# Performance work log

Measured on AMD Instinct MI355X. Metric: run time of the kernel, lower is better.

Reference implementation:

```python
import jax, jax.numpy as jnp
import numpy as np

LOG_2PI = float(np.log(2.0 * np.pi))


def kde_self_log_prob(X, sigma):
    """log prob of each row of X under a KDE whose components are all rows of X.

    Matches tfd.MixtureSameFamily(Categorical(uniform), MVNDiag(loc=X, scale=sigma)):
      log p(q) = logsumexp_i [ -0.5*||q - X_i||^2/sigma^2 - d*log(sigma) - d/2*log(2pi) ] - log(N)
    """
    n, d = X.shape
    sq = jnp.sum(X * X, axis=1)  # [N]
    # pairwise squared distances [N, N]; clamp tiny negatives from cancellation
    d2 = jnp.maximum(sq[:, None] + sq[None, :] - 2.0 * (X @ X.T), 0.0)
    log_comp = -0.5 * d2 / (sigma * sigma) - d * jnp.log(sigma) - 0.5 * d * LOG_2PI
    return jax.nn.logsumexp(log_comp, axis=1) - jnp.log(jnp.asarray(n, X.dtype))


def setup_inputs() -> dict:
    key = jax.random.key(0)
    kx, ky = jax.random.split(key)
    N, D = 8192, 128
    latent_x = jax.random.normal(kx, (N, D), dtype=jnp.float32)
    latent_y = jax.random.normal(ky, (N, D), dtype=jnp.float32)
    # learned bandwidth parameters (tf.Variable scalars, init 1.0)
    sigma_joint = jnp.float32(1.0)
    sigma_x = jnp.float32(1.0)
    sigma_y = jnp.float32(1.0)
    return {"latent_x": latent_x, "latent_y": latent_y,
            "sigma_joint": sigma_joint, "sigma_x": sigma_x, "sigma_y": sigma_y}


def reference(latent_x, latent_y, sigma_joint, sigma_x, sigma_y):
    latent_joint = jnp.concatenate([latent_x, latent_y], axis=1)  # [N, 2d]
    lp_joint = kde_self_log_prob(latent_joint, sigma_joint)  # [N]
    lp_x = kde_self_log_prob(latent_x, sigma_x)              # [N]
    lp_y = kde_self_log_prob(latent_y, sigma_y)              # [N]
    I_xy = jnp.exp(lp_joint) * (lp_joint - (lp_x + lp_y))
    return -jnp.sum(I_xy)
```

## Files before the change

kernel.cpp:

```cpp
#include <hip/hip_runtime.h>
#include <hip/hip_bf16.h>
#include <math.h>

#define NROW 8192
#define DD   128

#define V12BLK  512
#define V12NBLK 512
#define NRANKV8 8128

#define NT   64
#define TS   128
#define NPAIR 2080
#define FBLOCK 512

#define LOG_2PI 1.8378770664093453f
#define L2E     1.4426950408889634f
#define FP_SCALE 1099511627776.0

typedef __attribute__((ext_vector_type(8))) short bf16x8;
typedef __attribute__((ext_vector_type(4))) float f32x4;

#define SQX_B 0
#define SQY_B 32768
#define BSUM_B 65536
#define XB_B  65792
#define YB_B  (XB_B + NROW*DD*2)
#define TS_B  (YB_B + NROW*DD*2)
#define COLV8_B  TS_B
#define ROWSV8_B (COLV8_B + NRANKV8*192*4)
#define PS_B     (ROWSV8_B + 2048*192*4)
#define V8_NEED  (PS_B + 128*8*192*4)
#define ACC_B TS_B

__device__ __forceinline__ unsigned short f2bf(float f) {
    unsigned int x = __float_as_uint(f);
    unsigned int r = (x + 0x7fffu + ((x >> 16) & 1u)) >> 16;
    return (unsigned short)r;
}
__device__ __forceinline__ float fexp2(float x) { return __builtin_amdgcn_exp2f(x); }
__device__ __forceinline__ int rank_v8(int I, int J) {
    return I * 127 - (I * (I - 1)) / 2 + (J - I - 1);
}

template <bool PRE>
__global__ void sq_kernel(const float* __restrict__ X, const float* __restrict__ Y,
                          float* __restrict__ sqx, float* __restrict__ sqy,
                          unsigned short* __restrict__ XB, unsigned short* __restrict__ YB) {
    int tid  = threadIdx.x;
    int rowg = blockIdx.x * 8 + (tid >> 5);
    int lane = tid & 31;
    bool isX = rowg < NROW;
    const float* src = isX ? (X + (size_t)rowg * DD) : (Y + (size_t)(rowg - NROW) * DD);
    float4 v = reinterpret_cast<const float4*>(src)[lane];
    if (PRE) {
        unsigned int w0 = (unsigned int)f2bf(v.x) | ((unsigned int)f2bf(v.y) << 16);
        unsigned int w1 = (unsigned int)f2bf(v.z) | ((unsigned int)f2bf(v.w) << 16);
        unsigned short* dst = (isX ? XB + (size_t)rowg * DD
                                   : YB + (size_t)(rowg - NROW) * DD) + lane * 4;
        uint2 pk; pk.x = w0; pk.y = w1;
        *reinterpret_cast<uint2*>(dst) = pk;
    }
    float s = v.x * v.x + v.y * v.y + v.z * v.z + v.w * v.w;
#pragma unroll
    for (int m = 16; m; m >>= 1) s += __shfl_xor(s, m, 64);
    if (lane == 0) { if (isX) sqx[rowg] = s; else sqy[rowg - NROW] = s; }
}

template <bool SAME, bool DIAG>
__device__ __forceinline__ void combine_v8(const f32x4 (&ax)[4], const f32x4 (&ay)[4],
                                           const float* __restrict__ sqi0,
                                           const float* __restrict__ sqi1,
                                           float bxp, float byp,
                                           float cx2, float cy2, float m2cx, float m2cy,
                                           float rx, float ry,
                                           float (&prow)[4][4][3], float (&pcol)[3],
                                           int lane, int wql) {
    const int coll = wql * 16 + (lane & 15);
#pragma unroll
    for (int rf = 0; rf < 4; ++rf) {
        const int rb = rf * 16 + ((lane >> 4) << 2);
        f32x4 sixv = *reinterpret_cast<const f32x4*>(&sqi0[rb]);
        f32x4 siyv = *reinterpret_cast<const f32x4*>(&sqi1[rb]);
#pragma unroll
        for (int reg = 0; reg < 4; ++reg) {
            float tx = fmaf(ax[rf][reg], m2cx, fmaf(cx2, sixv[reg], bxp));
            float ty = fmaf(ay[rf][reg], m2cy, fmaf(cy2, siyv[reg], byp));
            float ex = fexp2(tx);
            float ey = fexp2(ty);
            float ej = SAME ? (ex * ey) : fexp2(fmaf(tx, rx, ty * ry));
            if (DIAG) {
                bool dg = (rb + reg) == coll;
                ex = dg ? 1.f : ex;  ey = dg ? 1.f : ey;  ej = dg ? 1.f : ej;
            }
            prow[rf][reg][0] += ex; prow[rf][reg][1] += ey; prow[rf][reg][2] += ej;
            pcol[0] += ex;          pcol[1] += ey;          pcol[2] += ej;
        }
    }
}

__launch_bounds__(V12BLK, 1)
__global__ void kde_v12(const unsigned short* __restrict__ XB,
                        const unsigned short* __restrict__ YB,
                        const float* __restrict__ sjp, const float* __restrict__ sxp,
                        const float* __restrict__ syp,
                        const float* __restrict__ sqx, const float* __restrict__ sqy,
                        float* __restrict__ COL, float* __restrict__ ROWS) {
    __shared__ unsigned short A[2][64][DD];
    __shared__ float sqi[2][64];
    __shared__ float rowred[8][64][3];

    const int tid  = threadIdx.x;
    const int lane = tid & 63;
    const int wq   = tid >> 6;
    const int wg   = wq >> 2;
    const int wql  = wq & 3;

    const int bid = blockIdx.x;
    const int cch = bid & 7;
    const int p   = bid >> 3;
    const int t0  = (129 * cch) >> 3;
    const int t1  = (129 * (cch + 1)) >> 3;
    const int nJA = 128 - p;

    const float sxv = *sxp, syv = *syp, sjv = *sjp;
    const float cx2 = -0.5f * L2E / (sxv * sxv);
    const float cy2 = -0.5f * L2E / (syv * syv);
    const float cj2 = -0.5f * L2E / (sjv * sjv);
    const bool  same = (cx2 == cy2) && (cy2 == cj2);
    const float m2cx = -2.f * cx2, m2cy = -2.f * cy2;
    const float rx = cj2 / cx2, ry = cj2 / cy2;

    float prow[4][4][3];
#pragma unroll
    for (int a = 0; a < 4; ++a)
#pragma unroll
        for (int b = 0; b < 4; ++b)
#pragma unroll
            for (int c = 0; c < 3; ++c) prow[a][b][c] = 0.f;

    int  prevWhich = -1;
    bool wrote0 = false, wrote1 = false;

    const int e1 = (t1 < nJA) ? t1 : nJA;
    const int s0 = (t0 > nJA) ? t0 : nJA;

    for (int band = 0; band < 2; ++band) {
        int I, Jf, cnt;
        if (band == 0) { I = p;       Jf = p + t0;  cnt = e1 - t0; }
        else           { I = 127 - p; Jf = s0 - 1;  cnt = t1 - s0; }
        if (cnt <= 0) continue;

        __syncthreads();
        if (prevWhich >= 0) {
#pragma unroll
            for (int rf = 0; rf < 4; ++rf)
#pragma unroll
                for (int reg = 0; reg < 4; ++reg)
#pragma unroll
                    for (int ch = 0; ch < 3; ++ch) {
                        float v = prow[rf][reg][ch];
                        v += __shfl_xor(v, 1, 64);
                        v += __shfl_xor(v, 2, 64);
                        v += __shfl_xor(v, 4, 64);
                        v += __shfl_xor(v, 8, 64);
                        if ((lane & 15) == 0)
                            rowred[wq][rf * 16 + ((lane >> 4) << 2) + reg][ch] = v;
                        prow[rf][reg][ch] = 0.f;
                    }
        }
        {
            int mat = wq >> 2;
            int g   = tid & 255;
            const unsigned short* gb = (mat ? YB : XB) + (size_t)(I * 64) * DD;
#pragma unroll
            for (int i = 0; i < 4; ++i) {
                int e    = g + i * 256;
                int row  = e >> 4;
                int col8 = e & 15;
                uint4 v = *reinterpret_cast<const uint4*>(gb + (size_t)row * DD + col8 * 8);
                int sl = col8 ^ (row & 7);
                *reinterpret_cast<uint4*>(&A[mat][row][sl * 8]) = v;
            }
        }
        if (tid < 128) sqi[tid >> 6][tid & 63] = ((tid < 64) ? sqx : sqy)[I * 64 + (tid & 63)];
        __syncthreads();
        if (prevWhich >= 0 && tid < 192) {
            int ch = tid >> 6, row = tid & 63;
            size_t slot = ((size_t)(p * 8 + cch) * 2 + prevWhich);
            float v = 0.f;
#pragma unroll
            for (int w = 0; w < 8; ++w) v += rowred[w][row][ch];
            ROWS[(slot * 3 + ch) * 64 + row] = v;
        }
        if (prevWhich == 0) wrote0 = true; else if (prevWhich == 1) wrote1 = true;
        prevWhich = (I == p) ? 0 : 1;

        for (int s = 0; s < cnt; s += 2) {
            const int  so    = s + wg;
            const bool valid = so < cnt;
            if (!valid) continue;
            const int J    = Jf + so;
            const bool diag = (I == J);
            const int colg = J * 64 + wql * 16 + (lane & 15);
            const float bxp = cx2 * sqx[colg];
            const float byp = cy2 * sqy[colg];

            f32x4 ax[4], ay[4];
#pragma unroll
            for (int rf = 0; rf < 4; ++rf) {
                ax[rf] = (f32x4){0.f, 0.f, 0.f, 0.f};
                ay[rf] = (f32x4){0.f, 0.f, 0.f, 0.f};
            }
#pragma unroll 2
            for (int kk = 0; kk < 4; ++kk) {
                bf16x8 bfx, bfy, afx[4], afy[4];
                {
                    size_t off = (size_t)colg * DD + kk * 32 + (lane >> 4) * 8;
                    bfx = *reinterpret_cast<const bf16x8*>(XB + off);
                    bfy = *reinterpret_cast<const bf16x8*>(YB + off);
                }
#pragma unroll
                for (int rf = 0; rf < 4; ++rf) {
                    int r  = rf * 16 + (lane & 15);
                    int sl = (kk * 4 + (lane >> 4)) ^ (r & 7);
                    afx[rf] = *reinterpret_cast<const bf16x8*>(&A[0][r][sl * 8]);
                    afy[rf] = *reinterpret_cast<const bf16x8*>(&A[1][r][sl * 8]);
                }
#pragma unroll
                for (int rf = 0; rf < 4; ++rf) {
                    ax[rf] = __builtin_amdgcn_mfma_f32_16x16x32_bf16(afx[rf], bfx, ax[rf], 0, 0, 0);
                    ay[rf] = __builtin_amdgcn_mfma_f32_16x16x32_bf16(afy[rf], bfy, ay[rf], 0, 0, 0);
                }
            }

            float pcol[3] = {0.f, 0.f, 0.f};
            if (same) { if (diag) combine_v8<true , true >(ax, ay, &sqi[0][0], &sqi[1][0], bxp, byp, cx2, cy2, m2cx, m2cy, rx, ry, prow, pcol, lane, wql);
                        else      combine_v8<true , false>(ax, ay, &sqi[0][0], &sqi[1][0], bxp, byp, cx2, cy2, m2cx, m2cy, rx, ry, prow, pcol, lane, wql); }
            else      { if (diag) combine_v8<false, true >(ax, ay, &sqi[0][0], &sqi[1][0], bxp, byp, cx2, cy2, m2cx, m2cy, rx, ry, prow, pcol, lane, wql);
                        else      combine_v8<false, false>(ax, ay, &sqi[0][0], &sqi[1][0], bxp, byp, cx2, cy2, m2cx, m2cy, rx, ry, prow, pcol, lane, wql); }

            if (!diag) {
                int rank = rank_v8(I, J);
#pragma unroll
                for (int ch = 0; ch < 3; ++ch) {
                    float v = pcol[ch];
                    v += __shfl_xor(v, 16, 64);
                    v += __shfl_xor(v, 32, 64);
                    if (lane < 16)
                        COL[((size_t)rank * 3 + ch) * 64 + wql * 16 + lane] = v;
                }
            }
        }
    }

    __syncthreads();
#pragma unroll
    for (int rf = 0; rf < 4; ++rf)
#pragma unroll
        for (int reg = 0; reg < 4; ++reg)
#pragma unroll
            for (int ch = 0; ch < 3; ++ch) {
                float v = prow[rf][reg][ch];
                v += __shfl_xor(v, 1, 64);
                v += __shfl_xor(v, 2, 64);
                v += __shfl_xor(v, 4, 64);
                v += __shfl_xor(v, 8, 64);
                if ((lane & 15) == 0)
                    rowred[wq][rf * 16 + ((lane >> 4) << 2) + reg][ch] = v;
            }
    __syncthreads();
    if (tid < 192) {
        int ch = tid >> 6, row = tid & 63;
        size_t slot = ((size_t)(p * 8 + cch) * 2 + prevWhich);
        float v = 0.f;
#pragma unroll
        for (int w = 0; w < 8; ++w) v += rowred[w][row][ch];
        ROWS[(slot * 3 + ch) * 64 + row] = v;
    }
    if (prevWhich == 0) wrote0 = true; else wrote1 = true;
    if (!wrote0 && tid < 192) {
        int ch = tid >> 6, row = tid & 63;
        ROWS[(((size_t)(p * 8 + cch) * 2 + 0) * 3 + ch) * 64 + row] = 0.f;
    }
    if (!wrote1 && tid < 192) {
        int ch = tid >> 6, row = tid & 63;
        ROWS[(((size_t)(p * 8 + cch) * 2 + 1) * 3 + ch) * 64 + row] = 0.f;
    }
}

__global__ void colsum_v8(const float* __restrict__ COL, float* __restrict__ PS) {
    const int J = blockIdx.x;
    const int s = blockIdx.y;
    const int t = threadIdx.x;
    const int i0 = (J * s) >> 3;
    const int i1 = (J * (s + 1)) >> 3;
    float v = 0.f;
    for (int I = i0; I < i1; ++I)
        v += COL[(size_t)rank_v8(I, J) * 192 + t];
    PS[((size_t)J * 8 + s) * 192 + t] = v;
}

__global__ void lp_v12(const float* __restrict__ sjp, const float* __restrict__ sxp,
                       const float* __restrict__ syp,
                       const float* __restrict__ PS, const float* __restrict__ ROWS,
                       float* __restrict__ bsum) {
    int b = blockIdx.x;
    int t = threadIdx.x;
    int r = b * 128 + t;
    int Ib = r >> 6;
    int c  = r & 63;
    float S0 = 0.f, S1 = 0.f, S2 = 0.f;
    {
        int p = (Ib < 64) ? Ib : 127 - Ib;
        int which = (Ib < 64) ? 0 : 1;
        for (int ch8 = 0; ch8 < 8; ++ch8) {
            size_t slot = ((size_t)(p * 8 + ch8) * 2 + which) * 3;
            S0 += ROWS[(slot + 0) * 64 + c];
            S1 += ROWS[(slot + 1) * 64 + c];
            S2 += ROWS[(slot + 2) * 64 + c];
        }
    }
    for (int s = 0; s < 8; ++s) {
        size_t base = ((size_t)Ib * 8 + s) * 192 + c;
        S0 += PS[base];
        S1 += PS[base + 64];
        S2 += PS[base + 128];
    }
    float sx = *sxp, sy = *syp, sj = *sjp;
    float logN = logf((float)NROW);
    float lpx = logf(S0) - (float)DD * logf(sx) - 0.5f * (float)DD * LOG_2PI - logN;
    float lpy = logf(S1) - (float)DD * logf(sy) - 0.5f * (float)DD * LOG_2PI - logN;
    float lpj = logf(S2) - 2.0f * (float)DD * logf(sj) - (float)DD * LOG_2PI - logN;
    float I_ = expf(lpj) * (lpj - lpx - lpy);
#pragma unroll
    for (int m = 1; m < 64; m <<= 1) I_ += __shfl_xor(I_, m, 64);
    __shared__ float w0s[2];
    if ((t & 63) == 0) w0s[t >> 6] = I_;
    __syncthreads();
    if (t == 0) bsum[b] = w0s[0] + w0s[1];
}

__global__ void final_reduce(const float* __restrict__ bsum, float* __restrict__ out) {
    int t = threadIdx.x;
    float v = bsum[t];
#pragma unroll
    for (int m = 1; m < 64; m <<= 1) v += __shfl_xor(v, m, 64);
    if (t == 0) out[0] = -v;
}

template <bool SAME>
__device__ __forceinline__ void fb_combine(const f32x4 (&ax)[4][2], const f32x4 (&ay)[4][2],
                                           const float (&sq)[4][TS],
                                           float (&rowred)[4][TS][3], float (&colred)[2][TS][3],
                                           int wr, int wc, int lane,
                                           float cx2, float cy2, float cj2) {
    float pcol[2][3] = {{0.f,0.f,0.f},{0.f,0.f,0.f}};
#pragma unroll
    for (int rf = 0; rf < 4; ++rf) {
        float prow[4][3] = {{0.f,0.f,0.f},{0.f,0.f,0.f},{0.f,0.f,0.f},{0.f,0.f,0.f}};
        float sxi[4], syi[4];
#pragma unroll
        for (int reg = 0; reg < 4; ++reg) {
            int row = wr*64 + rf*16 + ((lane>>4)<<2) + reg;
            sxi[reg] = sq[0][row]; syi[reg] = sq[1][row];
        }
#pragma unroll
        for (int cf = 0; cf < 2; ++cf) {
            int col = wc*32 + cf*16 + (lane & 15);
            float qx = sq[2][col], qy = sq[3][col];
#pragma unroll
            for (int reg = 0; reg < 4; ++reg) {
                float gx = ax[rf][cf][reg], gy = ay[rf][cf][reg];
                float d2x = fmaxf(fmaf(-2.f, gx, sxi[reg] + qx), 0.f);
                float d2y = fmaxf(fmaf(-2.f, gy, syi[reg] + qy), 0.f);
                float ex = fexp2(d2x * cx2);
                float ey = fexp2(d2y * cy2);
                float ej = SAME ? (ex * ey) : fexp2(fmaf(d2y, cj2, d2x * cj2));
                prow[reg][0] += ex; prow[reg][1] += ey; prow[reg][2] += ej;
                pcol[cf][0]  += ex; pcol[cf][1]  += ey; pcol[cf][2]  += ej;
            }
        }
#pragma unroll
        for (int reg = 0; reg < 4; ++reg)
#pragma unroll
            for (int ch = 0; ch < 3; ++ch) {
                float v = prow[reg][ch];
                v += __shfl_xor(v, 1, 64); v += __shfl_xor(v, 2, 64);
                v += __shfl_xor(v, 4, 64); v += __shfl_xor(v, 8, 64);
                if ((lane & 15) == 0)
                    rowred[wc][wr*64 + rf*16 + ((lane>>4)<<2) + reg][ch] = v;
            }
    }
#pragma unroll
    for (int cf = 0; cf < 2; ++cf)
#pragma unroll
        for (int ch = 0; ch < 3; ++ch) {
            float v = pcol[cf][ch];
            v += __shfl_xor(v, 16, 64); v += __shfl_xor(v, 32, 64);
            if (lane < 16) colred[wr][wc*32 + cf*16 + lane][ch] = v;
        }
}

__launch_bounds__(FBLOCK)
__global__ void kde_fb(const float* __restrict__ X, const float* __restrict__ Y,
                       const float* __restrict__ sjp, const float* __restrict__ sxp,
                       const float* __restrict__ syp,
                       unsigned long long* __restrict__ acc,
                       const float* __restrict__ sqx, const float* __restrict__ sqy) {
    __shared__ unsigned short T[4][TS][DD];
    __shared__ float sq[4][TS];
    __shared__ float rowred[4][TS][3];
    __shared__ float colred[2][TS][3];

    const int tid  = threadIdx.x;
    const int lane = tid & 63;
    const int wid  = tid >> 6;
    const int wr   = wid >> 2;
    const int wc   = wid & 3;

    int b = (blockIdx.x & 7) * (NPAIR / 8) + (blockIdx.x >> 3);
    int ti = 0, rem = b;
    while (rem >= NT - ti) { rem -= NT - ti; ++ti; }
    int tj = ti + rem;
    const int i0 = ti * TS, j0 = tj * TS;

    const float sxv = *sxp, syv = *syp, sjv = *sjp;
    const float cx2 = -0.5f * L2E / (sxv * sxv);
    const float cy2 = -0.5f * L2E / (syv * syv);
    const float cj2 = -0.5f * L2E / (sjv * sjv);
    const bool samesig = (cx2 == cy2) && (cy2 == cj2);

    for (int c = tid; c < 8192; c += FBLOCK) {
        int t = c >> 11, row = (c >> 4) & 127, col8 = c & 15;
        const float* base =
            (t == 0) ? X + (size_t)i0 * DD : (t == 1) ? Y + (size_t)i0 * DD :
            (t == 2) ? X + (size_t)j0 * DD : Y + (size_t)j0 * DD;
        const float4* s4 = reinterpret_cast<const float4*>(base + row * DD + col8 * 8);
        float4 a = s4[0], bb = s4[1];
        unsigned int w0 = (unsigned int)f2bf(a.x)  | ((unsigned int)f2bf(a.y)  << 16);
        unsigned int w1 = (unsigned int)f2bf(a.z)  | ((unsigned int)f2bf(a.w)  << 16);
        unsigned int w2 = (unsigned int)f2bf(bb.x) | ((unsigned int)f2bf(bb.y) << 16);
        unsigned int w3 = (unsigned int)f2bf(bb.z) | ((unsigned int)f2bf(bb.w) << 16);
        uint4 pk = make_uint4(w0, w1, w2, w3);
        int sl = (col8 ^ (row & 7)) << 3;
        *reinterpret_cast<uint4*>(&T[t][row][sl]) = pk;
    }
    {
        int t = tid >> 7, r = tid & 127;
        const float* s = (t == 0) ? sqx + i0 : (t == 1) ? sqy + i0
                       : (t == 2) ? sqx + j0 : sqy + j0;
        sq[t][r] = s[r];
    }
    __syncthreads();

    f32x4 ax[4][2], ay[4][2];
#pragma unroll
    for (int rf = 0; rf < 4; ++rf)
#pragma unroll
        for (int cf = 0; cf < 2; ++cf) {
            ax[rf][cf] = (f32x4){0.f,0.f,0.f,0.f};
            ay[rf][cf] = (f32x4){0.f,0.f,0.f,0.f};
        }
#pragma unroll
    for (int kk = 0; kk < 4; ++kk) {
        const int k0 = kk * 4 + (lane >> 4);
        bf16x8 afx[4], afy[4], bfx[2], bfy[2];
#pragma unroll
        for (int rf = 0; rf < 4; ++rf) {
            int r  = wr * 64 + rf * 16 + (lane & 15);
            int sl = (k0 ^ (r & 7)) << 3;
            afx[rf] = *reinterpret_cast<const bf16x8*>(&T[0][r][sl]);
            afy[rf] = *reinterpret_cast<const bf16x8*>(&T[1][r][sl]);
        }
#pragma unroll
        for (int cf = 0; cf < 2; ++cf) {
            int r  = wc * 32 + cf * 16 + (lane & 15);
            int sl = (k0 ^ (r & 7)) << 3;
            bfx[cf] = *reinterpret_cast<const bf16x8*>(&T[2][r][sl]);
            bfy[cf] = *reinterpret_cast<const bf16x8*>(&T[3][r][sl]);
        }
#pragma unroll
        for (int rf = 0; rf < 4; ++rf)
#pragma unroll
            for (int cf = 0; cf < 2; ++cf) {
                ax[rf][cf] = __builtin_amdgcn_mfma_f32_16x16x32_bf16(afx[rf], bfx[cf], ax[rf][cf], 0, 0, 0);
                ay[rf][cf] = __builtin_amdgcn_mfma_f32_16x16x32_bf16(afy[rf], bfy[cf], ay[rf][cf], 0, 0, 0);
            }
    }

    if (samesig) fb_combine<true >(ax, ay, sq, rowred, colred, wr, wc, lane, cx2, cy2, cj2);
    else         fb_combine<false>(ax, ay, sq, rowred, colred, wr, wc, lane, cx2, cy2, cj2);
    __syncthreads();

    if (tid < TS) {
        int r = tid;
#pragma unroll
        for (int ch = 0; ch < 3; ++ch) {
            float v = rowred[0][r][ch] + rowred[1][r][ch] + rowred[2][r][ch] + rowred[3][r][ch];
            atomicAdd(&acc[(size_t)(i0 + r) * 3 + ch],
                      (unsigned long long)(long long)((double)v * FP_SCALE));
        }
    } else if (tid < 2 * TS && ti != tj) {
        int r = tid - TS;
#pragma unroll
        for (int ch = 0; ch < 3; ++ch) {
            float v = colred[0][r][ch] + colred[1][r][ch];
            atomicAdd(&acc[(size_t)(j0 + r) * 3 + ch],
                      (unsigned long long)(long long)((double)v * FP_SCALE));
        }
    }
}

__global__ void lp_fb(const float* __restrict__ sjp, const float* __restrict__ sxp,
                      const float* __restrict__ syp,
                      const unsigned long long* __restrict__ acc,
                      float* __restrict__ bsum) {
    int b = blockIdx.x, t = threadIdx.x;
    size_t row = (size_t)b * 128 + t;
    const double INV = 1.0 / FP_SCALE;
    float S0 = (float)((double)acc[row * 3 + 0] * INV);
    float S1 = (float)((double)acc[row * 3 + 1] * INV);
    float S2 = (float)((double)acc[row * 3 + 2] * INV);
    float sx = *sxp, sy = *syp, sj = *sjp;
    float logN = logf((float)NROW);
    float lpx = logf(S0) - (float)DD * logf(sx) - 0.5f * (float)DD * LOG_2PI - logN;
    float lpy = logf(S1) - (float)DD * logf(sy) - 0.5f * (float)DD * LOG_2PI - logN;
    float lpj = logf(S2) - 2.0f * (float)DD * logf(sj) - (float)DD * LOG_2PI - logN;
    float I = expf(lpj) * (lpj - lpx - lpy);
#pragma unroll
    for (int m = 1; m < 64; m <<= 1) I += __shfl_xor(I, m, 64);
    __shared__ float w0[2];
    if ((t & 63) == 0) w0[t >> 6] = I;
    __syncthreads();
    if (t == 0) bsum[b] = w0[0] + w0[1];
}

extern "C" void kernel_launch(void* const* d_in, const int* in_sizes, int n_in,
                              void* d_out, int out_size, void* d_ws, size_t ws_size,
                              hipStream_t stream) {
    (void)in_sizes; (void)n_in; (void)out_size;
    const float* X  = (const float*)d_in[0];
    const float* Y  = (const float*)d_in[1];
    const float* sj = (const float*)d_in[2];
    const float* sx = (const float*)d_in[3];
    const float* sy = (const float*)d_in[4];
    float* out = (float*)d_out;
    char*  w   = (char*)d_ws;

    float* SQX  = (float*)(w + SQX_B);
    float* SQY  = (float*)(w + SQY_B);
    float* BSUM = (float*)(w + BSUM_B);
    unsigned short* XB = (unsigned short*)(w + XB_B);
    unsigned short* YB = (unsigned short*)(w + YB_B);

    if (ws_size >= (size_t)V8_NEED) {
        float* COLS = (float*)(w + COLV8_B);
        float* ROWS = (float*)(w + ROWSV8_B);
        float* PS   = (float*)(w + PS_B);
        sq_kernel<true ><<<dim3(2048), dim3(256), 0, stream>>>(X, Y, SQX, SQY, XB, YB);
        kde_v12<<<dim3(V12NBLK), dim3(V12BLK), 0, stream>>>(XB, YB, sj, sx, sy, SQX, SQY, COLS, ROWS);
        colsum_v8<<<dim3(128, 8), dim3(192), 0, stream>>>(COLS, PS);
        lp_v12<<<dim3(64), dim3(128), 0, stream>>>(sj, sx, sy, PS, ROWS, BSUM);
    } else {
        unsigned long long* ACC = (unsigned long long*)(w + ACC_B);
        hipMemsetAsync(w + ACC_B, 0, NROW * 3 * sizeof(unsigned long long), stream);
        sq_kernel<false><<<dim3(2048), dim3(256), 0, stream>>>(X, Y, SQX, SQY, XB, YB);
        kde_fb<<<dim3(NPAIR), dim3(FBLOCK), 0, stream>>>(X, Y, sj, sx, sy, ACC, SQX, SQY);
        lp_fb<<<dim3(64), dim3(128), 0, stream>>>(sj, sx, sy, ACC, BSUM);
    }
    final_reduce<<<dim3(1), dim3(64), 0, stream>>>(BSUM, out);
}
```

Baseline: 89.38 us.

## Switch pairwise KDE tiles to 32x32x16 bf16 MFMA with atomic column sums

The main pairwise kernel now computes each 64x64 tile as four 32x32 quadrants using 32x32x16 bf16 MFMA instructions instead of sixteen 16x16x32 MFMAs per wave. This cuts B-fragment and LDS loads per accumulated element and changes the row and column partial-sum layout. Two waves now cover each column block, so column partials go to COL through atomicAdd, which requires a new memset of the COL buffer before launch. The exchange is extra atomics and a memset, plus a different register footprint.

```diff
diff --git a/kernel.cpp b/kernel.cpp
--- a/kernel.cpp
+++ b/kernel.cpp
@@ -5,8 +5,8 @@
 #define NROW 8192
 #define DD   128
 
-#define V12BLK  512
-#define V12NBLK 512
+#define V13BLK  512
+#define V13NBLK 512
 #define NRANKV8 8128
 
 #define NT   64
@@ -18,8 +18,9 @@
 #define L2E     1.4426950408889634f
 #define FP_SCALE 1099511627776.0
 
-typedef __attribute__((ext_vector_type(8))) short bf16x8;
-typedef __attribute__((ext_vector_type(4))) float f32x4;
+typedef __attribute__((ext_vector_type(8)))  short bf16x8;
+typedef __attribute__((ext_vector_type(4)))  float f32x4;
+typedef __attribute__((ext_vector_type(16))) float f32x16;
 
 #define SQX_B 0
 #define SQY_B 32768
@@ -67,40 +68,41 @@
     if (lane == 0) { if (isX) sqx[rowg] = s; else sqy[rowg - NROW] = s; }
 }
 
+
 template <bool SAME, bool DIAG>
-__device__ __forceinline__ void combine_v8(const f32x4 (&ax)[4], const f32x4 (&ay)[4],
-                                           const float* __restrict__ sqi0,
-                                           const float* __restrict__ sqi1,
-                                           float bxp, float byp,
-                                           float cx2, float cy2, float m2cx, float m2cy,
-                                           float rx, float ry,
-                                           float (&prow)[4][4][3], float (&pcol)[3],
-                                           int lane, int wql) {
-    const int coll = wql * 16 + (lane & 15);
-#pragma unroll
-    for (int rf = 0; rf < 4; ++rf) {
-        const int rb = rf * 16 + ((lane >> 4) << 2);
-        f32x4 sixv = *reinterpret_cast<const f32x4*>(&sqi0[rb]);
-        f32x4 siyv = *reinterpret_cast<const f32x4*>(&sqi1[rb]);
-#pragma unroll
-        for (int reg = 0; reg < 4; ++reg) {
-            float tx = fmaf(ax[rf][reg], m2cx, fmaf(cx2, sixv[reg], bxp));
-            float ty = fmaf(ay[rf][reg], m2cy, fmaf(cy2, siyv[reg], byp));
+__device__ __forceinline__ void combine_v13(const f32x16& axv, const f32x16& ayv,
+                                            const float* __restrict__ sq0,
+                                            const float* __restrict__ sq1,
+                                            float bxp, float byp,
+                                            float cx2, float cy2, float m2cx, float m2cy,
+                                            float rx, float ry,
+                                            int qr, int qc, int hi, int c32,
+                                            float (&prow)[16][3], float (&pcol)[3]) {
+#pragma unroll
+    for (int q = 0; q < 4; ++q) {
+        const int rb = qr * 32 + q * 8 + hi * 4;
+        f32x4 sixv = *reinterpret_cast<const f32x4*>(&sq0[rb]);
+        f32x4 siyv = *reinterpret_cast<const f32x4*>(&sq1[rb]);
+#pragma unroll
+        for (int m = 0; m < 4; ++m) {
+            const int reg = q * 4 + m;
+            float tx = fmaf(axv[reg], m2cx, fmaf(cx2, sixv[m], bxp));
+            float ty = fmaf(ayv[reg], m2cy, fmaf(cy2, siyv[m], byp));
             float ex = fexp2(tx);
             float ey = fexp2(ty);
             float ej = SAME ? (ex * ey) : fexp2(fmaf(tx, rx, ty * ry));
             if (DIAG) {
-                bool dg = (rb + reg) == coll;
+                bool dg = (qr == qc) && ((q * 8 + hi * 4 + m) == c32);
                 ex = dg ? 1.f : ex;  ey = dg ? 1.f : ey;  ej = dg ? 1.f : ej;
             }
-            prow[rf][reg][0] += ex; prow[rf][reg][1] += ey; prow[rf][reg][2] += ej;
-            pcol[0] += ex;          pcol[1] += ey;          pcol[2] += ej;
-        }
-    }
-}
-
-__launch_bounds__(V12BLK, 1)
-__global__ void kde_v12(const unsigned short* __restrict__ XB,
+            prow[reg][0] += ex; prow[reg][1] += ey; prow[reg][2] += ej;
+            pcol[0] += ex;      pcol[1] += ey;      pcol[2] += ej;
+        }
+    }
+}
+
+__launch_bounds__(V13BLK, 1)
+__global__ void kde_v13(const unsigned short* __restrict__ XB,
                         const unsigned short* __restrict__ YB,
                         const float* __restrict__ sjp, const float* __restrict__ sxp,
                         const float* __restrict__ syp,
@@ -108,13 +110,17 @@
                         float* __restrict__ COL, float* __restrict__ ROWS) {
     __shared__ unsigned short A[2][64][DD];
     __shared__ float sqi[2][64];
-    __shared__ float rowred[8][64][3];
+    __shared__ float rowred[8][32][3];
 
     const int tid  = threadIdx.x;
     const int lane = tid & 63;
     const int wq   = tid >> 6;
     const int wg   = wq >> 2;
     const int wql  = wq & 3;
+    const int qr   = wql >> 1;
+    const int qc   = wql & 1;
+    const int hi   = lane >> 5;
+    const int c32  = lane & 31;
 
     const int bid = blockIdx.x;
     const int cch = bid & 7;
@@ -131,13 +137,11 @@
     const float m2cx = -2.f * cx2, m2cy = -2.f * cy2;
     const float rx = cj2 / cx2, ry = cj2 / cy2;
 
-    float prow[4][4][3];
-#pragma unroll
-    for (int a = 0; a < 4; ++a)
-#pragma unroll
-        for (int b = 0; b < 4; ++b)
-#pragma unroll
-            for (int c = 0; c < 3; ++c) prow[a][b][c] = 0.f;
+    float prow[16][3];
+#pragma unroll
+    for (int a = 0; a < 16; ++a)
+#pragma unroll
+        for (int c = 0; c < 3; ++c) prow[a][c] = 0.f;
 
     int  prevWhich = -1;
     bool wrote0 = false, wrote1 = false;
@@ -154,19 +158,20 @@
         __syncthreads();
         if (prevWhich >= 0) {
 #pragma unroll
-            for (int rf = 0; rf < 4; ++rf)
-#pragma unroll
-                for (int reg = 0; reg < 4; ++reg)
+            for (int q = 0; q < 4; ++q)
+#pragma unroll
+                for (int m = 0; m < 4; ++m)
 #pragma unroll
                     for (int ch = 0; ch < 3; ++ch) {
-                        float v = prow[rf][reg][ch];
+                        float v = prow[q * 4 + m][ch];
                         v += __shfl_xor(v, 1, 64);
                         v += __shfl_xor(v, 2, 64);
                         v += __shfl_xor(v, 4, 64);
                         v += __shfl_xor(v, 8, 64);
-                        if ((lane & 15) == 0)
-                            rowred[wq][rf * 16 + ((lane >> 4) << 2) + reg][ch] = v;
-                        prow[rf][reg][ch] = 0.f;
+                        v += __shfl_xor(v, 16, 64);
+                        if ((lane & 31) == 0)
+                            rowred[wq][q * 8 + hi * 4 + m][ch] = v;
+                        prow[q * 4 + m][ch] = 0.f;
                     }
         }
         {
@@ -187,11 +192,11 @@
         __syncthreads();
         if (prevWhich >= 0 && tid < 192) {
             int ch = tid >> 6, row = tid & 63;
+            int q2 = row >> 5, rl = row & 31;
             size_t slot = ((size_t)(p * 8 + cch) * 2 + prevWhich);
-            float v = 0.f;
-#pragma unroll
-            for (int w = 0; w < 8; ++w) v += rowred[w][row][ch];
-            ROWS[(slot * 3 + ch) * 64 + row] = v;
+            ROWS[(slot * 3 + ch) * 64 + row] =
+                rowred[q2 * 2 + 0][rl][ch] + rowred[q2 * 2 + 1][rl][ch] +
+                rowred[4 + q2 * 2 + 0][rl][ch] + rowred[4 + q2 * 2 + 1][rl][ch];
         }
         if (prevWhich == 0) wrote0 = true; else if (prevWhich == 1) wrote1 = true;
         prevWhich = (I == p) ? 0 : 1;
@@ -202,53 +207,42 @@
             if (!valid) continue;
             const int J    = Jf + so;
             const bool diag = (I == J);
-            const int colg = J * 64 + wql * 16 + (lane & 15);
+            const int colg = J * 64 + qc * 32 + c32;
             const float bxp = cx2 * sqx[colg];
             const float byp = cy2 * sqy[colg];
 
-            f32x4 ax[4], ay[4];
-#pragma unroll
-            for (int rf = 0; rf < 4; ++rf) {
-                ax[rf] = (f32x4){0.f, 0.f, 0.f, 0.f};
-                ay[rf] = (f32x4){0.f, 0.f, 0.f, 0.f};
-            }
+            f32x16 axv, ayv;
+#pragma unroll
+            for (int i = 0; i < 16; ++i) { axv[i] = 0.f; ayv[i] = 0.f; }
+
+            const int r64   = qr * 32 + c32;
+            const int rmask = r64 & 7;
+            const unsigned short* pbx = XB + (size_t)colg * DD + hi * 8;
+            const unsigned short* pby = YB + (size_t)colg * DD + hi * 8;
 #pragma unroll 2
-            for (int kk = 0; kk < 4; ++kk) {
-                bf16x8 bfx, bfy, afx[4], afy[4];
-                {
-                    size_t off = (size_t)colg * DD + kk * 32 + (lane >> 4) * 8;
-                    bfx = *reinterpret_cast<const bf16x8*>(XB + off);
-                    bfy = *reinterpret_cast<const bf16x8*>(YB + off);
-                }
-#pragma unroll
-                for (int rf = 0; rf < 4; ++rf) {
-                    int r  = rf * 16 + (lane & 15);
-                    int sl = (kk * 4 + (lane >> 4)) ^ (r & 7);
-                    afx[rf] = *reinterpret_cast<const bf16x8*>(&A[0][r][sl * 8]);
-                    afy[rf] = *reinterpret_cast<const bf16x8*>(&A[1][r][sl * 8]);
-                }
-#pragma unroll
-                for (int rf = 0; rf < 4; ++rf) {
-                    ax[rf] = __builtin_amdgcn_mfma_f32_16x16x32_bf16(afx[rf], bfx, ax[rf], 0, 0, 0);
-                    ay[rf] = __builtin_amdgcn_mfma_f32_16x16x32_bf16(afy[rf], bfy, ay[rf], 0, 0, 0);
-                }
+            for (int ks = 0; ks < 8; ++ks) {
+                bf16x8 bfx = *reinterpret_cast<const bf16x8*>(pbx + ks * 16);
+                bf16x8 bfy = *reinterpret_cast<const bf16x8*>(pby + ks * 16);
+                int sl = (ks * 2 + hi) ^ rmask;
+                bf16x8 afx = *reinterpret_cast<const bf16x8*>(&A[0][r64][sl * 8]);
+                bf16x8 afy = *reinterpret_cast<const bf16x8*>(&A[1][r64][sl * 8]);
+                axv = __builtin_amdgcn_mfma_f32_32x32x16_bf16(afx, bfx, axv, 0, 0, 0);
+                ayv = __builtin_amdgcn_mfma_f32_32x32x16_bf16(afy, bfy, ayv, 0, 0, 0);
             }
 
             float pcol[3] = {0.f, 0.f, 0.f};
-            if (same) { if (diag) combine_v8<true , true >(ax, ay, &sqi[0][0], &sqi[1][0], bxp, byp, cx2, cy2, m2cx, m2cy, rx, ry, prow, pcol, lane, wql);
-                        else      combine_v8<true , false>(ax, ay, &sqi[0][0], &sqi[1][0], bxp, byp, cx2, cy2, m2cx, m2cy, rx, ry, prow, pcol, lane, wql); }
-            else      { if (diag) combine_v8<false, true >(ax, ay, &sqi[0][0], &sqi[1][0], bxp, byp, cx2, cy2, m2cx, m2cy, rx, ry, prow, pcol, lane, wql);
-                        else      combine_v8<false, false>(ax, ay, &sqi[0][0], &sqi[1][0], bxp, byp, cx2, cy2, m2cx, m2cy, rx, ry, prow, pcol, lane, wql); }
+            if (same) { if (diag) combine_v13<true , true >(axv, ayv, &sqi[0][0], &sqi[1][0], bxp, byp, cx2, cy2, m2cx, m2cy, rx, ry, qr, qc, hi, c32, prow, pcol);
+                        else      combine_v13<true , false>(axv, ayv, &sqi[0][0], &sqi[1][0], bxp, byp, cx2, cy2, m2cx, m2cy, rx, ry, qr, qc, hi, c32, prow, pcol); }
+            else      { if (diag) combine_v13<false, true >(axv, ayv, &sqi[0][0], &sqi[1][0], bxp, byp, cx2, cy2, m2cx, m2cy, rx, ry, qr, qc, hi, c32, prow, pcol);
+                        else      combine_v13<false, false>(axv, ayv, &sqi[0][0], &sqi[1][0], bxp, byp, cx2, cy2, m2cx, m2cy, rx, ry, qr, qc, hi, c32, prow, pcol); }
 
             if (!diag) {
                 int rank = rank_v8(I, J);
 #pragma unroll
                 for (int ch = 0; ch < 3; ++ch) {
-                    float v = pcol[ch];
-                    v += __shfl_xor(v, 16, 64);
-                    v += __shfl_xor(v, 32, 64);
-                    if (lane < 16)
-                        COL[((size_t)rank * 3 + ch) * 64 + wql * 16 + lane] = v;
+                    float v = pcol[ch] + __shfl_xor(pcol[ch], 32, 64);
+                    if (hi == 0)
+                        atomicAdd(&COL[((size_t)rank * 3 + ch) * 64 + qc * 32 + c32], v);
                 }
             }
         }
@@ -256,27 +250,28 @@
 
     __syncthreads();
 #pragma unroll
-    for (int rf = 0; rf < 4; ++rf)
-#pragma unroll
-        for (int reg = 0; reg < 4; ++reg)
+    for (int q = 0; q < 4; ++q)
+#pragma unroll
+        for (int m = 0; m < 4; ++m)
 #pragma unroll
             for (int ch = 0; ch < 3; ++ch) {
-                float v = prow[rf][reg][ch];
+                float v = prow[q * 4 + m][ch];
                 v += __shfl_xor(v, 1, 64);
                 v += __shfl_xor(v, 2, 64);
                 v += __shfl_xor(v, 4, 64);
                 v += __shfl_xor(v, 8, 64);
-                if ((lane & 15) == 0)
-                    rowred[wq][rf * 16 + ((lane >> 4) << 2) + reg][ch] = v;
+                v += __shfl_xor(v, 16, 64);
+                if ((lane & 31) == 0)
+                    rowred[wq][q * 8 + hi * 4 + m][ch] = v;
             }
     __syncthreads();
     if (tid < 192) {
         int ch = tid >> 6, row = tid & 63;
+        int q2 = row >> 5, rl = row & 31;
         size_t slot = ((size_t)(p * 8 + cch) * 2 + prevWhich);
-        float v = 0.f;
-#pragma unroll
-        for (int w = 0; w < 8; ++w) v += rowred[w][row][ch];
-        ROWS[(slot * 3 + ch) * 64 + row] = v;
+        ROWS[(slot * 3 + ch) * 64 + row] =
+            rowred[q2 * 2 + 0][rl][ch] + rowred[q2 * 2 + 1][rl][ch] +
+            rowred[4 + q2 * 2 + 0][rl][ch] + rowred[4 + q2 * 2 + 1][rl][ch];
     }
     if (prevWhich == 0) wrote0 = true; else wrote1 = true;
     if (!wrote0 && tid < 192) {
@@ -301,7 +296,7 @@
     PS[((size_t)J * 8 + s) * 192 + t] = v;
 }
 
-__global__ void lp_v12(const float* __restrict__ sjp, const float* __restrict__ sxp,
+__global__ void lp_v13(const float* __restrict__ sjp, const float* __restrict__ sxp,
                        const float* __restrict__ syp,
                        const float* __restrict__ PS, const float* __restrict__ ROWS,
                        float* __restrict__ bsum) {
@@ -558,10 +553,11 @@
         float* COLS = (float*)(w + COLV8_B);
         float* ROWS = (float*)(w + ROWSV8_B);
         float* PS   = (float*)(w + PS_B);
+        hipMemsetAsync(w + COLV8_B, 0, (size_t)NRANKV8 * 192 * 4, stream);
         sq_kernel<true ><<<dim3(2048), dim3(256), 0, stream>>>(X, Y, SQX, SQY, XB, YB);
-        kde_v12<<<dim3(V12NBLK), dim3(V12BLK), 0, stream>>>(XB, YB, sj, sx, sy, SQX, SQY, COLS, ROWS);
+        kde_v13<<<dim3(V13NBLK), dim3(V13BLK), 0, stream>>>(XB, YB, sj, sx, sy, SQX, SQY, COLS, ROWS);
         colsum_v8<<<dim3(128, 8), dim3(192), 0, stream>>>(COLS, PS);
-        lp_v12<<<dim3(64), dim3(128), 0, stream>>>(sj, sx, sy, PS, ROWS, BSUM);
+        lp_v13<<<dim3(64), dim3(128), 0, stream>>>(sj, sx, sy, PS, ROWS, BSUM);
     } else {
         unsigned long long* ACC = (unsigned long long*)(w + ACC_B);
         hipMemsetAsync(w + ACC_B, 0, NROW * 3 * sizeof(unsigned long long), stream);
```

Result: slower. 129.1 us (+44.5%).
